# Kernel optimization log

Hardware: AMD Instinct MI355X
Metric: run time of the kernel (lower is better)

## Reference

```python
import jax, jax.numpy as jnp
import numpy as np

TEMP = 0.1
THRESH = 0.9
HARD_RATIO = 0.5
B = 8192
K = max(1, int(B * HARD_RATIO))  # 4096 hard negatives per row


def _normalize(x):
    return x / jnp.linalg.norm(x, axis=-1, keepdims=True)


def _projector(x, W1, b1, W2, b2):
    # Linear -> ReLU -> Linear
    h = jax.nn.relu(x @ W1 + b1)
    return h @ W2 + b2


def _hard_negative_mining(sim):
    bsz = sim.shape[0]
    eye = jnp.eye(bsz, dtype=bool)
    neg_sim = jnp.where(eye, -jnp.inf, sim)
    noise = (neg_sim > THRESH / TEMP) & ~eye
    ranking = jnp.where(noise, -jnp.inf, neg_sim)
    _, idx = jax.lax.top_k(ranking, K)  # (B, K) hard negative indices
    hard = jnp.zeros((bsz, bsz), dtype=bool).at[jnp.arange(bsz)[:, None], idx].set(True)
    # noise weight (0.5) overrides hard weight (1.5), as in torch sequential assignment
    w = jnp.where(noise, 0.5, jnp.where(hard, 1.5, 1.0)).astype(sim.dtype)
    return sim * w


def _modal_loss(id_emb, feat, Wa, ba, W1, b1, W2, b2, mw):
    modal_feat = feat @ Wa + ba                       # adapter
    modal_proj = _normalize(_projector(modal_feat, W1, b1, W2, b2))
    id_proj = _normalize(_projector(id_emb, W1, b1, W2, b2))
    sim = (id_proj @ modal_proj.T) / TEMP             # (B, B)
    sim = _hard_negative_mining(sim)
    ce = -jnp.diagonal(jax.nn.log_softmax(sim, axis=-1))  # labels = arange
    return jnp.mean(ce * mw)


def setup_inputs() -> dict:
    key = jax.random.key(0)
    ks = jax.random.split(key, 20)
    HID, PROJ = 1024, 512

    def lin(k, i, o):
        return (jax.random.normal(k, (i, o), jnp.float32) / np.sqrt(i)).astype(jnp.float32)

    return {
        'id_embeddings': jax.random.normal(ks[0], (B, HID), jnp.float32),
        'text_feat': jax.random.normal(ks[1], (B, 768), jnp.float32),
        'visual_feat': jax.random.normal(ks[2], (B, 2048), jnp.float32),
        'modal_weights': jax.random.uniform(ks[3], (B, 2), jnp.float32),
        'Wa_t': lin(ks[4], 768, HID),  'ba_t': jnp.zeros((HID,), jnp.float32),
        'Wa_v': lin(ks[5], 2048, HID), 'ba_v': jnp.zeros((HID,), jnp.float32),
        'W1_t': lin(ks[6], HID, HID),  'b1_t': jnp.zeros((HID,), jnp.float32),
        'W2_t': lin(ks[7], HID, PROJ), 'b2_t': jnp.zeros((PROJ,), jnp.float32),
        'W1_v': lin(ks[8], HID, HID),  'b1_v': jnp.zeros((HID,), jnp.float32),
        'W2_v': lin(ks[9], HID, PROJ), 'b2_v': jnp.zeros((PROJ,), jnp.float32),
    }


def reference(id_embeddings, text_feat, visual_feat, modal_weights,
              Wa_t, ba_t, Wa_v, ba_v,
              W1_t, b1_t, W2_t, b2_t,
              W1_v, b1_v, W2_v, b2_v):
    # sorted(modal_features.keys()) -> ['text', 'visual'] (idx 0, 1)
    l_text = _modal_loss(id_embeddings, text_feat, Wa_t, ba_t, W1_t, b1_t, W2_t, b2_t, modal_weights[:, 0])
    l_vis = _modal_loss(id_embeddings, visual_feat, Wa_v, ba_v, W1_v, b1_v, W2_v, b2_v, modal_weights[:, 1])
    return (l_text + l_vis) / 2.0
```

## Files before the change

kernel.cpp:

```cpp
#include <hip/hip_runtime.h>
#include <math.h>
#include <stdint.h>


typedef __attribute__((ext_vector_type(4))) float  floatx4;
typedef __attribute__((ext_vector_type(8))) __bf16 bf16x8;

__device__ __forceinline__ unsigned short f2bf(float f)
{
    unsigned u = __float_as_uint(f);
    unsigned r = (u + 0x7FFFu + ((u >> 16) & 1u)) >> 16;
    return (unsigned short)r;
}

__device__ __forceinline__ float bf2f(unsigned short u)
{
    return __uint_as_float((unsigned)u << 16);
}

__device__ __forceinline__ void gld_lds16(const void* g, void* l)
{
    __builtin_amdgcn_global_load_lds(
        (const __attribute__((address_space(1))) void*)g,
        (__attribute__((address_space(3))) void*)(uint32_t)(uintptr_t)l,
        16, 0, 0);
}

#define EPW 136

__device__ __forceinline__ void stage_tile(
    const unsigned short* __restrict__ g, int ld, int k0,
    unsigned short* lds, int t)
{
#pragma unroll
    for (int it = 0; it < 4; ++it) {
        const int row = it * 32 + (t >> 3);
        const int c   = (t & 7) ^ ((t >> 3) & 7);
        gld_lds16(g + (size_t)row * ld + k0 + c * 8,
                  lds + (it * 256 + t) * 8);
    }
}

__global__ __launch_bounds__(256) void gemm_bt_mfma(
    const unsigned short* __restrict__ A, int lda,
    const unsigned short* __restrict__ B, int ldb,
    unsigned short* __restrict__ C, int ldc, int M, int N, int K,
    const float* __restrict__ bias, int relu, float scale)
{
    __shared__ __align__(16) unsigned short smem[32768];

    const int num_n = N >> 7;
    const int per   = gridDim.x >> 3;
    const int pid   = blockIdx.x;
    const int npid  = (pid & 7) * per + (pid >> 3);
    const int width = 4 * num_n;
    const int group = npid / width;
    const int rem   = npid - group * width;
    const int pm    = group * 4 + (rem & 3);
    const int pn    = rem >> 2;

    const int t    = threadIdx.x;
    const int lane = t & 63;
    const int w    = t >> 6;
    const int wr   = w >> 1;
    const int wc   = w & 1;
    const size_t m0 = (size_t)pm * 128;
    const size_t n0 = (size_t)pn * 128;

    floatx4 acc[4][4] = {};

    const unsigned short* Abase = A + m0 * (size_t)lda;
    const unsigned short* Bbase = B + n0 * (size_t)ldb;

    int aoff[4][2], boff[4][2];
#pragma unroll
    for (int i = 0; i < 4; ++i) {
        const int ra = wr * 64 + i * 16 + (lane & 15);
        const int rb = wc * 64 + i * 16 + (lane & 15);
#pragma unroll
        for (int ks = 0; ks < 2; ++ks) {
            const int cc = ks * 4 + (lane >> 4);
            aoff[i][ks] = ra * 64 + ((cc ^ (ra & 7)) << 3);
            boff[i][ks] = rb * 64 + ((cc ^ (rb & 7)) << 3);
        }
    }

    const int NT = K >> 6;

    stage_tile(Abase, lda, 0, smem, t);
    stage_tile(Bbase, ldb, 0, smem + 8192, t);

    int cur = 0;
    for (int kt = 0; kt < NT; ++kt) {
        if (kt + 1 < NT) {
            unsigned short* nb = smem + (cur ^ 1) * 16384;
            stage_tile(Abase, lda, (kt + 1) << 6, nb, t);
            stage_tile(Bbase, ldb, (kt + 1) << 6, nb + 8192, t);
            asm volatile("s_waitcnt vmcnt(8)" ::: "memory");
        } else {
            asm volatile("s_waitcnt vmcnt(0)" ::: "memory");
        }
        __builtin_amdgcn_sched_barrier(0);
        __builtin_amdgcn_s_barrier();
        __builtin_amdgcn_sched_barrier(0);

        const unsigned short* As = smem + cur * 16384;
        const unsigned short* Bs = As + 8192;

        bf16x8 af[4][2], bfr[4][2];
#pragma unroll
        for (int i = 0; i < 4; ++i) {
#pragma unroll
            for (int ks = 0; ks < 2; ++ks) {
                af[i][ks]  = *(const bf16x8*)(As + aoff[i][ks]);
                bfr[i][ks] = *(const bf16x8*)(Bs + boff[i][ks]);
            }
        }
#pragma unroll
        for (int i = 0; i < 4; ++i)
#pragma unroll
            for (int j = 0; j < 4; ++j)
#pragma unroll
                for (int ks = 0; ks < 2; ++ks)
                    acc[i][j] = __builtin_amdgcn_mfma_f32_16x16x32_bf16(
                        af[i][ks], bfr[j][ks], acc[i][j], 0, 0, 0);

        asm volatile("s_waitcnt lgkmcnt(0)" ::: "memory");
        __builtin_amdgcn_sched_barrier(0);
        __builtin_amdgcn_s_barrier();
        __builtin_amdgcn_sched_barrier(0);
        cur ^= 1;
    }

    const int col   = lane & 15;
    const int rquad = (lane >> 4) * 4;
#pragma unroll
    for (int j = 0; j < 4; ++j) {
        const int lc = wc * 64 + j * 16 + col;
        const float bv = bias ? bias[n0 + lc] : 0.0f;
#pragma unroll
        for (int i = 0; i < 4; ++i) {
            const int lr0 = wr * 64 + i * 16 + rquad;
#pragma unroll
            for (int r = 0; r < 4; ++r) {
                float v = acc[i][j][r] * scale + bv;
                if (relu) v = fmaxf(v, 0.0f);
                smem[(lr0 + r) * EPW + lc] = f2bf(v);
            }
        }
    }
    __syncthreads();
#pragma unroll
    for (int h = 0; h < 2; ++h) {
        const int cr = h * 64 + (t >> 2);
        const int cq = t & 3;
#pragma unroll
        for (int q = 0; q < 4; ++q) {
            const int chunk = cq + q * 4;
            uint4 v = *(const uint4*)(smem + cr * EPW + chunk * 8);
            *(uint4*)(C + (m0 + cr) * (size_t)ldc + n0 + chunk * 8) = v;
        }
    }
}

__global__ __launch_bounds__(256) void cast_bf16_kernel(
    const float* __restrict__ in, unsigned short* __restrict__ out, int n4)
{
    const int i = blockIdx.x * 256 + threadIdx.x;
    if (i < n4) {
        float4 v = *(const float4*)(in + (size_t)i * 4);
        ushort4 o;
        o.x = f2bf(v.x); o.y = f2bf(v.y); o.z = f2bf(v.z); o.w = f2bf(v.w);
        *(ushort4*)(out + (size_t)i * 4) = o;
    }
}

__global__ __launch_bounds__(256) void transpose_cast_kernel(
    const float* __restrict__ W, unsigned short* __restrict__ WT, int K, int N)
{
    __shared__ float tile[32][33];
    const int k0 = blockIdx.y * 32;
    const int n0 = blockIdx.x * 32;
    const int tr = threadIdx.x >> 3;
    const int tc = (threadIdx.x & 7) * 4;

    float4 v = *(const float4*)(W + (size_t)(k0 + tr) * N + n0 + tc);
    tile[tr][tc + 0] = v.x;
    tile[tr][tc + 1] = v.y;
    tile[tr][tc + 2] = v.z;
    tile[tr][tc + 3] = v.w;
    __syncthreads();

    ushort4 o;
    o.x = f2bf(tile[tc + 0][tr]);
    o.y = f2bf(tile[tc + 1][tr]);
    o.z = f2bf(tile[tc + 2][tr]);
    o.w = f2bf(tile[tc + 3][tr]);
    *(ushort4*)(WT + (size_t)(n0 + tr) * K + k0 + tc) = o;
}

__global__ __launch_bounds__(128) void normalize_bf16_kernel(
    unsigned short* __restrict__ X)
{
    const int r = blockIdx.x;
    const int t = threadIdx.x;
    unsigned short* row = X + (size_t)r * 512;
    ushort4 u = *(const ushort4*)(row + t * 4);
    float x0 = bf2f(u.x), x1 = bf2f(u.y), x2 = bf2f(u.z), x3 = bf2f(u.w);
    float ss = x0 * x0 + x1 * x1 + x2 * x2 + x3 * x3;
#pragma unroll
    for (int off = 32; off > 0; off >>= 1) ss += __shfl_down(ss, off, 64);
    __shared__ float sred[2];
    if ((t & 63) == 0) sred[t >> 6] = ss;
    __syncthreads();
    float inv = 1.0f / sqrtf(sred[0] + sred[1]);
    ushort4 o;
    o.x = f2bf(x0 * inv); o.y = f2bf(x1 * inv);
    o.z = f2bf(x2 * inv); o.w = f2bf(x3 * inv);
    *(ushort4*)(row + t * 4) = o;
}

__global__ __launch_bounds__(256, 4) void row_loss_kernel(
    const unsigned short* __restrict__ S, int row_base,
    const float* __restrict__ mw, int midx, float* __restrict__ accum)
{
    __shared__ unsigned hist[4096];
    __shared__ unsigned wtot[4];
    __shared__ float fred[4];
    __shared__ unsigned sh_b;
    __shared__ float sh_diag;

    const int t    = threadIdx.x;
    const int lane = t & 63;
    const int wv   = t >> 6;
    const int i    = row_base + blockIdx.x;
    const unsigned short* Srow = S + (size_t)blockIdx.x * 8192;

    for (int b = t; b < 4096; b += 256) hist[b] = 0;

    uint4 raw[4];
#pragma unroll
    for (int seg = 0; seg < 4; ++seg)
        raw[seg] = *(const uint4*)(Srow + seg * 2048 + t * 8);
    __syncthreads();

#pragma unroll
    for (int seg = 0; seg < 4; ++seg) {
        const unsigned short* e = (const unsigned short*)&raw[seg];
#pragma unroll
        for (int q = 0; q < 8; ++q) {
            const int j = seg * 2048 + t * 8 + q;
            const float s = bf2f(e[q]);
            if (j != i && s <= 9.0f) {
                int k = (int)((s + 10.25f) * 200.0f);
                k = k < 1 ? 1 : (k > 4095 ? 4095 : k);
                atomicAdd(&hist[k], 1u);
            }
        }
    }
    __syncthreads();

    unsigned local = 0;
#pragma unroll
    for (int q = 0; q < 16; ++q) local += hist[t * 16 + q];
    unsigned suf = local;
#pragma unroll
    for (int off = 1; off < 64; off <<= 1) {
        unsigned v = __shfl_down(suf, off, 64);
        if (lane + off < 64) suf += v;
    }
    if (lane == 0) wtot[wv] = suf;
    __syncthreads();
    unsigned wsuf = 0;
#pragma unroll
    for (int q = 0; q < 4; ++q) wsuf += (q > wv) ? wtot[q] : 0u;
    suf += wsuf;

    const unsigned target = 4096;
    const unsigned above  = suf - local;
    if (suf >= target && above < target) {
        unsigned cum = above;
        int bsel = t * 16;
#pragma unroll
        for (int q = 15; q >= 0; --q) {
            unsigned c = hist[t * 16 + q];
            if (cum + c >= target) { bsel = t * 16 + q; break; }
            cum += c;
        }
        sh_b = (unsigned)bsel;
    }
    if (t == 0 && suf < target) sh_b = 1u;
    __syncthreads();
    const unsigned bsel = sh_b;

    float lsum = 0.0f;
#pragma unroll
    for (int seg = 0; seg < 4; ++seg) {
        const unsigned short* e = (const unsigned short*)&raw[seg];
#pragma unroll
        for (int q = 0; q < 8; ++q) {
            const int j = seg * 2048 + t * 8 + q;
            const float s = bf2f(e[q]);
            bool diag  = (j == i);
            bool noise = (!diag && s > 9.0f);
            int k = (int)((s + 10.25f) * 200.0f);
            k = k < 1 ? 1 : (k > 4095 ? 4095 : k);
            bool hard = !diag && !noise && ((unsigned)k >= bsel);
            float wgt = noise ? 0.5f : (hard ? 1.5f : 1.0f);
            float ws = s * wgt;
            if (diag) sh_diag = ws;
            lsum += __expf(ws - 16.0f);
        }
    }
#pragma unroll
    for (int off = 32; off > 0; off >>= 1)
        lsum += __shfl_down(lsum, off, 64);
    if (lane == 0) fred[wv] = lsum;
    __syncthreads();
    if (t == 0) {
        float total = fred[0] + fred[1] + fred[2] + fred[3];
        float lse = 16.0f + logf(total);
        float ce = lse - sh_diag;
        atomicAdd(&accum[midx * 64 + (blockIdx.x & 63)],
                  ce * mw[(size_t)i * 2 + midx]);
    }
}

__global__ void zero_kernel(float* __restrict__ accum)
{
    if (threadIdx.x < 128) accum[threadIdx.x] = 0.0f;
}

__global__ void finalize_kernel(const float* __restrict__ accum,
                                float* __restrict__ out)
{
    float s = 0.0f;
    for (int q = 0; q < 128; ++q) s += accum[q];
    out[0] = s * (1.0f / 16384.0f);
}

extern "C" void kernel_launch(void* const* d_in, const int* in_sizes, int n_in,
                              void* d_out, int out_size, void* d_ws, size_t ws_size,
                              hipStream_t stream)
{
    (void)in_sizes; (void)n_in; (void)out_size; (void)ws_size;

    const float* id_emb = (const float*)d_in[0];
    const float* feats[2] = { (const float*)d_in[1], (const float*)d_in[2] };
    const float* mw     = (const float*)d_in[3];
    const float* Wa[2]  = { (const float*)d_in[4],  (const float*)d_in[6]  };
    const float* ba[2]  = { (const float*)d_in[5],  (const float*)d_in[7]  };
    const float* W1[2]  = { (const float*)d_in[8],  (const float*)d_in[12] };
    const float* b1[2]  = { (const float*)d_in[9],  (const float*)d_in[13] };
    const float* W2[2]  = { (const float*)d_in[10], (const float*)d_in[14] };
    const float* b2[2]  = { (const float*)d_in[11], (const float*)d_in[15] };
    const int    Fdim[2] = { 768, 2048 };

    char* p = (char*)d_ws;
    unsigned short* WaT   = (unsigned short*)p; p += (size_t)1024 * 2048 * 2;
    unsigned short* W1T   = (unsigned short*)p; p += (size_t)1024 * 1024 * 2;
    unsigned short* W2T   = (unsigned short*)p; p += (size_t)512  * 1024 * 2;
    unsigned short* X     = (unsigned short*)p; p += (size_t)16384 * 1024 * 2;
    unsigned short* featb = (unsigned short*)p; p += (size_t)8192 * 2048 * 2;
    unsigned short* H     = (unsigned short*)p; p += (size_t)16384 * 1024 * 2;
    unsigned short* PB    = (unsigned short*)p; p += (size_t)16384 * 512  * 2;
    float*          accum = (float*)p;
    unsigned short* S     = featb;

    zero_kernel<<<1, 128, 0, stream>>>(accum);

    cast_bf16_kernel<<<(8192 * 1024 / 4 + 255) / 256, 256, 0, stream>>>(
        id_emb, X + (size_t)8192 * 1024, 8192 * 1024 / 4);

    for (int m = 0; m < 2; ++m) {
        const int F = Fdim[m];

        cast_bf16_kernel<<<(8192 * F / 4 + 255) / 256, 256, 0, stream>>>(
            feats[m], featb, 8192 * F / 4);
        transpose_cast_kernel<<<dim3(1024 / 32, F / 32), 256, 0, stream>>>(
            Wa[m], WaT, F, 1024);
        transpose_cast_kernel<<<dim3(1024 / 32, 1024 / 32), 256, 0, stream>>>(
            W1[m], W1T, 1024, 1024);
        transpose_cast_kernel<<<dim3(512 / 32, 1024 / 32), 256, 0, stream>>>(
            W2[m], W2T, 1024, 512);

        gemm_bt_mfma<<<(8192 / 128) * (1024 / 128), 256, 0, stream>>>(
            featb, F, WaT, F, X, 1024, 8192, 1024, F, ba[m], 0, 1.0f);

        gemm_bt_mfma<<<(16384 / 128) * (1024 / 128), 256, 0, stream>>>(
            X, 1024, W1T, 1024, H, 1024, 16384, 1024, 1024, b1[m], 1, 1.0f);
        gemm_bt_mfma<<<(16384 / 128) * (512 / 128), 256, 0, stream>>>(
            H, 1024, W2T, 1024, PB, 512, 16384, 512, 1024, b2[m], 0, 1.0f);
        normalize_bf16_kernel<<<16384, 128, 0, stream>>>(PB);

        const unsigned short* mproj = PB;
        const unsigned short* iproj = PB + (size_t)8192 * 512;

        for (int c = 0; c < 2; ++c) {
            gemm_bt_mfma<<<(4096 / 128) * (8192 / 128), 256, 0, stream>>>(
                iproj + (size_t)c * 4096 * 512, 512, mproj, 512,
                S, 8192, 4096, 8192, 512, nullptr, 0, 10.0f);
            row_loss_kernel<<<4096, 256, 0, stream>>>(
                S, c * 4096, mw, m, accum);
        }
    }

    finalize_kernel<<<1, 1, 0, stream>>>(accum, (float*)d_out);
}
```

Baseline: 707.5 us.

## Add 256x256-tile 512-thread MFMA GEMM for W1 projection and similarity GEMMs

Introduces a new bf16 GEMM kernel with 256x256 output tiles, 8 waves per block and a double-buffered 64-wide K loop. B-tile loads are split so they overlap the first half of the MFMA work. The epilogue is staged through LDS in two halves. Larger tiles raise arithmetic intensity and cut global reloads for the W1 and similarity GEMMs. The cost is a 128KB LDS footprint and high register pressure, which may limit occupancy (launch bound 512,2) and leave fewer blocks per wave of CUs.

```diff
diff --git a/kernel.cpp b/kernel.cpp
--- a/kernel.cpp
+++ b/kernel.cpp
@@ -26,7 +26,172 @@
         16, 0, 0);
 }
 
-#define EPW 136
+#define EPW  136
+#define EPW2 264
+
+
+__device__ __forceinline__ void stage_half256(
+    const unsigned short* __restrict__ g, int ld, int k0,
+    unsigned short* lds, int t)
+{
+#pragma unroll
+    for (int it = 0; it < 2; ++it) {
+        const int li  = it * 512 + t;
+        const int row = li >> 3;
+        const int c   = (li & 7) ^ (row & 7);
+        gld_lds16(g + (size_t)row * ld + k0 + c * 8, lds + li * 8);
+    }
+}
+
+__global__ __launch_bounds__(512, 2) void gemm_bt_256(
+    const unsigned short* __restrict__ A, int lda,
+    const unsigned short* __restrict__ B, int ldb,
+    unsigned short* __restrict__ C, int ldc, int M, int N, int K,
+    const float* __restrict__ bias, int relu, float scale)
+{
+    __shared__ __align__(16) unsigned short smem[65536];
+
+    const int num_n = N >> 8;
+    const int per   = gridDim.x >> 3;
+    const int pid   = blockIdx.x;
+    const int npid  = (pid & 7) * per + (pid >> 3);
+    const int width = 4 * num_n;
+    const int group = npid / width;
+    const int rem   = npid - group * width;
+    const int pm    = group * 4 + (rem & 3);
+    const int pn    = rem >> 2;
+
+    const int t    = threadIdx.x;
+    const int lane = t & 63;
+    const int w    = t >> 6;
+    const int wr   = w >> 2;
+    const int wc   = w & 3;
+    const size_t m0 = (size_t)pm * 256;
+    const size_t n0 = (size_t)pn * 256;
+
+    floatx4 acc[8][4] = {};
+
+    const unsigned short* Abase = A + m0 * (size_t)lda;
+    const unsigned short* Bbase = B + n0 * (size_t)ldb;
+
+    int aoff[8][2], boff[4][2];
+#pragma unroll
+    for (int ks = 0; ks < 2; ++ks) {
+        const int cc = ks * 4 + (lane >> 4);
+#pragma unroll
+        for (int i = 0; i < 8; ++i) {
+            const int rr = i * 16 + (lane & 15);
+            aoff[i][ks] = wr * 8192 + rr * 64 + ((cc ^ (rr & 7)) << 3);
+        }
+#pragma unroll
+        for (int j = 0; j < 4; ++j) {
+            const int rb = wc * 64 + j * 16 + (lane & 15);
+            const int rr = rb & 127;
+            boff[j][ks] = 16384 + (rb >> 7) * 8192 + rr * 64
+                        + ((cc ^ (rr & 7)) << 3);
+        }
+    }
+
+    const int NT = K >> 6;
+
+    stage_half256(Abase, lda, 0, smem, t);
+    stage_half256(Abase + (size_t)128 * lda, lda, 0, smem + 8192, t);
+    stage_half256(Bbase, ldb, 0, smem + 16384, t);
+    stage_half256(Bbase + (size_t)128 * ldb, ldb, 0, smem + 24576, t);
+
+    for (int kt = 0; kt < NT; ++kt) {
+        unsigned short* cb = smem + (kt & 1) * 32768;
+        unsigned short* nb = smem + ((kt + 1) & 1) * 32768;
+        const int kn = (kt + 1) << 6;
+
+        if (kt + 1 < NT) {
+            stage_half256(Abase, lda, kn, nb, t);
+            stage_half256(Abase + (size_t)128 * lda, lda, kn, nb + 8192, t);
+            asm volatile("s_waitcnt vmcnt(4)" ::: "memory");
+        } else {
+            asm volatile("s_waitcnt vmcnt(0)" ::: "memory");
+        }
+        __builtin_amdgcn_sched_barrier(0);
+        __builtin_amdgcn_s_barrier();
+        __builtin_amdgcn_sched_barrier(0);
+
+        {
+            bf16x8 af[8], bf[4];
+#pragma unroll
+            for (int i = 0; i < 8; ++i) af[i] = *(const bf16x8*)(cb + aoff[i][0]);
+#pragma unroll
+            for (int j = 0; j < 4; ++j) bf[j] = *(const bf16x8*)(cb + boff[j][0]);
+            __builtin_amdgcn_s_setprio(1);
+#pragma unroll
+            for (int i = 0; i < 8; ++i)
+#pragma unroll
+                for (int j = 0; j < 4; ++j)
+                    acc[i][j] = __builtin_amdgcn_mfma_f32_16x16x32_bf16(
+                        af[i], bf[j], acc[i][j], 0, 0, 0);
+            __builtin_amdgcn_s_setprio(0);
+        }
+        __builtin_amdgcn_sched_barrier(0);
+        __builtin_amdgcn_s_barrier();
+        __builtin_amdgcn_sched_barrier(0);
+
+        if (kt + 1 < NT) {
+            stage_half256(Bbase, ldb, kn, nb + 16384, t);
+            stage_half256(Bbase + (size_t)128 * ldb, ldb, kn, nb + 24576, t);
+        }
+        {
+            bf16x8 af[8], bf[4];
+#pragma unroll
+            for (int i = 0; i < 8; ++i) af[i] = *(const bf16x8*)(cb + aoff[i][1]);
+#pragma unroll
+            for (int j = 0; j < 4; ++j) bf[j] = *(const bf16x8*)(cb + boff[j][1]);
+            __builtin_amdgcn_s_setprio(1);
+#pragma unroll
+            for (int i = 0; i < 8; ++i)
+#pragma unroll
+                for (int j = 0; j < 4; ++j)
+                    acc[i][j] = __builtin_amdgcn_mfma_f32_16x16x32_bf16(
+                        af[i], bf[j], acc[i][j], 0, 0, 0);
+            __builtin_amdgcn_s_setprio(0);
+        }
+        __builtin_amdgcn_sched_barrier(0);
+        __builtin_amdgcn_s_barrier();
+        __builtin_amdgcn_sched_barrier(0);
+    }
+
+    const int col   = lane & 15;
+    const int rquad = (lane >> 4) * 4;
+#pragma unroll
+    for (int h = 0; h < 2; ++h) {
+        if (wr == h) {
+#pragma unroll
+            for (int j = 0; j < 4; ++j) {
+                const int lc = wc * 64 + j * 16 + col;
+                const float bv = bias ? bias[n0 + lc] : 0.0f;
+#pragma unroll
+                for (int i = 0; i < 8; ++i) {
+                    const int lr0 = i * 16 + rquad;
+#pragma unroll
+                    for (int r = 0; r < 4; ++r) {
+                        float v = acc[i][j][r] * scale + bv;
+                        if (relu) v = fmaxf(v, 0.0f);
+                        smem[(lr0 + r) * EPW2 + lc] = f2bf(v);
+                    }
+                }
+            }
+        }
+        __syncthreads();
+        const int cr = t >> 2;
+        const int cq = t & 3;
+#pragma unroll
+        for (int q = 0; q < 8; ++q) {
+            const int chunk = cq + q * 4;
+            uint4 v = *(const uint4*)(smem + cr * EPW2 + chunk * 8);
+            *(uint4*)(C + (m0 + h * 128 + cr) * (size_t)ldc + n0 + chunk * 8) = v;
+        }
+        __syncthreads();
+    }
+}
+
 
 __device__ __forceinline__ void stage_tile(
     const unsigned short* __restrict__ g, int ld, int k0,
@@ -387,7 +552,7 @@
         gemm_bt_mfma<<<(8192 / 128) * (1024 / 128), 256, 0, stream>>>(
             featb, F, WaT, F, X, 1024, 8192, 1024, F, ba[m], 0, 1.0f);
 
-        gemm_bt_mfma<<<(16384 / 128) * (1024 / 128), 256, 0, stream>>>(
+        gemm_bt_256<<<(16384 / 256) * (1024 / 256), 512, 0, stream>>>(
             X, 1024, W1T, 1024, H, 1024, 16384, 1024, 1024, b1[m], 1, 1.0f);
         gemm_bt_mfma<<<(16384 / 128) * (512 / 128), 256, 0, stream>>>(
             H, 1024, W2T, 1024, PB, 512, 16384, 512, 1024, b2[m], 0, 1.0f);
@@ -397,7 +562,7 @@
         const unsigned short* iproj = PB + (size_t)8192 * 512;
 
         for (int c = 0; c < 2; ++c) {
-            gemm_bt_mfma<<<(4096 / 128) * (8192 / 128), 256, 0, stream>>>(
+            gemm_bt_256<<<(4096 / 256) * (8192 / 256), 512, 0, stream>>>(
                 iproj + (size_t)c * 4096 * 512, 512, mproj, 512,
                 S, 8192, 4096, 8192, 512, nullptr, 0, 10.0f);
             row_loss_kernel<<<4096, 256, 0, stream>>>(
```

Measured after the change: 688.5 us. -2.7%, faster.
